# Kernel tuning notes

Measured on AMD Instinct MI355X. Metric: run time of the kernel, lower is better.

## Reference

```python
import jax, jax.numpy as jnp
import numpy as np

L, H, NH, FF = 12, 768, 12, 3072
HD = H // NH
B, T = 8, 512
SCALE = 1.0 / float(np.sqrt(HD))
EPS = 1e-12


def setup_inputs() -> dict:
    key = jax.random.key(0)
    ks = jax.random.split(key, 10)
    s = jnp.float32(0.02)

    def p(k, shape):
        return jax.random.normal(k, shape, dtype=jnp.float32) * s

    return {
        "hidden_states": jax.random.normal(ks[0], (B, T, H), dtype=jnp.float32),
        "attention_mask": jnp.ones((B, T), dtype=jnp.float32),
        "Wq": p(ks[1], (L, H, H)), "bq": jnp.zeros((L, H), jnp.float32),
        "Wk": p(ks[2], (L, H, H)), "bk": jnp.zeros((L, H), jnp.float32),
        "Wv": p(ks[3], (L, H, H)), "bv": jnp.zeros((L, H), jnp.float32),
        "Wao": p(ks[4], (L, H, H)), "bao": jnp.zeros((L, H), jnp.float32),
        "ln1_g": jnp.ones((L, H), jnp.float32), "ln1_b": jnp.zeros((L, H), jnp.float32),
        "Wi": p(ks[5], (L, H, FF)), "bi": jnp.zeros((L, FF), jnp.float32),
        "Wo": p(ks[6], (L, FF, H)), "bo": jnp.zeros((L, H), jnp.float32),
        "ln2_g": jnp.ones((L, H), jnp.float32), "ln2_b": jnp.zeros((L, H), jnp.float32),
    }


def _layernorm(x, g, b):
    m = jnp.mean(x, axis=-1, keepdims=True)
    v = jnp.mean((x - m) ** 2, axis=-1, keepdims=True)
    return (x - m) * jax.lax.rsqrt(v + EPS) * g + b


def _encoder(hidden_states, attention_mask, params):
    # additive mask: (1 - mask) * -10000, broadcast to [B, 1, 1, T]
    add_mask = (1.0 - attention_mask)[:, None, None, :] * -10000.0

    def layer(x, p):
        wq, bq, wk, bk, wv, bv, wao, bao, g1, b1, wi, bi, wo, bo, g2, b2 = p
        q = (x @ wq + bq).reshape(B, T, NH, HD)
        k = (x @ wk + bk).reshape(B, T, NH, HD)
        v = (x @ wv + bv).reshape(B, T, NH, HD)
        scores = jnp.einsum('bihd,bjhd->bhij', q, k) * SCALE + add_mask
        probs = jax.nn.softmax(scores, axis=-1)  # dropout p=0 (eval)
        ctx = jnp.einsum('bhij,bjhd->bihd', probs, v).reshape(B, T, H)
        attn_out = _layernorm(ctx @ wao + bao + x, g1, b1)
        ff = jax.nn.gelu(attn_out @ wi + bi, approximate=False)
        out = _layernorm(ff @ wo + bo + attn_out, g2, b2)
        return out, None

    out, _ = jax.lax.scan(layer, hidden_states, params)
    return out


def reference(hidden_states, attention_mask, Wq, bq, Wk, bk, Wv, bv, Wao, bao,
              ln1_g, ln1_b, Wi, bi, Wo, bo, ln2_g, ln2_b):
    params = (Wq, bq, Wk, bk, Wv, bv, Wao, bao, ln1_g, ln1_b, Wi, bi, Wo, bo, ln2_g, ln2_b)
    return _encoder(hidden_states, attention_mask, params)
```

## Files before the change

### kernel.cpp

```cpp
#include <hip/hip_runtime.h>
#include <hip/hip_bf16.h>

typedef __bf16 bf16;
typedef __attribute__((ext_vector_type(8))) __bf16 bf16x8;
typedef __attribute__((ext_vector_type(4))) float f32x4;

#define MFMA16(a, b, c) __builtin_amdgcn_mfma_f32_16x16x32_bf16((a), (b), (c), 0, 0, 0)

__device__ __forceinline__ void async16(const bf16* g, bf16* l) {
    __builtin_amdgcn_global_load_lds((__attribute__((address_space(1))) void*)(g),
                                     (__attribute__((address_space(3))) void*)(l), 16, 0, 0);
}

__device__ __forceinline__ void xcd_swizzle(int& bx, int& by, int& bz) {
    const int gx = gridDim.x, gy = gridDim.y;
    const int nwg = gx * gy * gridDim.z;
    const int lin = blockIdx.x + gx * (blockIdx.y + gy * blockIdx.z);
    const int xcd = lin & 7, seq = lin >> 3;
    const int q = nwg >> 3, r = nwg & 7;
    const int nl = (xcd < r ? xcd * (q + 1) : r * (q + 1) + (xcd - r) * q) + seq;
    bx = nl % gx;
    const int t = nl / gx;
    by = t % gy;
    bz = t / gy;
}

template <int MODE, int BM>
__global__ __launch_bounds__(256) void gemm_kernel(
    const bf16* __restrict__ A, const bf16* __restrict__ WT,
    const float* __restrict__ b0, const float* __restrict__ b1, const float* __restrict__ b2,
    int s1, int s2,
    void* __restrict__ o0, void* __restrict__ o1,
    int N, int K, int Kpart)
{
    constexpr int MT = BM / 32;
    __shared__ __align__(16) bf16 sA[2][BM * 32];
    __shared__ __align__(16) bf16 sB[2][128 * 32];

    const int tid  = threadIdx.x;
    const int lane = tid & 63;
    const int wave = tid >> 6;
    const int quad = lane >> 4;
    const int l15  = lane & 15;
    const int wm   = (wave >> 1) * (BM / 2);
    const int wn   = (wave & 1) * 64;

    int bxs, bys, bzs;
    xcd_swizzle(bxs, bys, bzs);
    const int bm = bys * BM;
    const int bn = bxs * 128;
    const int kbase = bzs * Kpart;

    f32x4 acc[MT][4];
#pragma unroll
    for (int i = 0; i < MT; i++)
#pragma unroll
        for (int j = 0; j < 4; j++)
#pragma unroll
            for (int r = 0; r < 4; r++) acc[i][j][r] = 0.0f;

    const int idx1 = tid + 256;
    const int ra0 = tid  >> 2, ca0 = (tid  & 3) * 8;
    const int rb1 = idx1 >> 2, cb1 = (idx1 & 3) * 8;

    const bf16* Arow0 = A  + (size_t)(bm + ra0) * K + kbase + ca0;
    const bf16* Arow1 = A  + (size_t)(bm + rb1) * K + kbase + cb1;
    const bf16* Brow0 = WT + (size_t)(bn + ra0) * K + kbase + ca0;
    const bf16* Brow1 = WT + (size_t)(bn + rb1) * K + kbase + cb1;

    const int nk = Kpart >> 5;

    async16(Arow0, sA[0] + tid * 8);
    if (BM == 128) async16(Arow1, sA[0] + idx1 * 8);
    async16(Brow0, sB[0] + tid * 8);
    async16(Brow1, sB[0] + idx1 * 8);
    __syncthreads();

    int cur = 0;
    for (int kt = 0; kt < nk; kt++) {
        if (kt + 1 < nk) {
            const int ko = (kt + 1) * 32;
            async16(Arow0 + ko, sA[cur ^ 1] + tid * 8);
            if (BM == 128) async16(Arow1 + ko, sA[cur ^ 1] + idx1 * 8);
            async16(Brow0 + ko, sB[cur ^ 1] + tid * 8);
            async16(Brow1 + ko, sB[cur ^ 1] + idx1 * 8);
        }
        bf16x8 af[MT], bfr[4];
#pragma unroll
        for (int i = 0; i < MT; i++)
            af[i] = *(const bf16x8*)(sA[cur] + (wm + i * 16 + l15) * 32 + quad * 8);
#pragma unroll
        for (int i = 0; i < 4; i++)
            bfr[i] = *(const bf16x8*)(sB[cur] + (wn + i * 16 + l15) * 32 + quad * 8);
#pragma unroll
        for (int mt = 0; mt < MT; mt++)
#pragma unroll
            for (int nt = 0; nt < 4; nt++)
                acc[mt][nt] = MFMA16(af[mt], bfr[nt], acc[mt][nt]);
        __syncthreads();
        cur ^= 1;
    }

    void* outp = (bzs == 0) ? o0 : o1;

#pragma unroll
    for (int nt = 0; nt < 4; nt++) {
        const int col = bn + wn + nt * 16 + l15;
        float bias = 0.0f;
        if (MODE != 1)
            bias = (col < s1) ? b0[col] : (col < s2) ? b1[col - s1] : b2[col - s2];
#pragma unroll
        for (int mt = 0; mt < MT; mt++) {
#pragma unroll
            for (int r = 0; r < 4; r++) {
                const int row = bm + wm + mt * 16 + quad * 4 + r;
                float v = acc[mt][nt][r] + bias;
                if (MODE == 2) v = 0.5f * v * (1.0f + erff(v * 0.70710678118654752f));
                if (MODE == 1) ((float*)outp)[(size_t)row * N + col] = v;
                else           ((bf16*)outp)[(size_t)row * N + col] = (bf16)v;
            }
        }
    }
}

__global__ __launch_bounds__(256) void vtrans_kernel(
    const bf16* __restrict__ qkv, bf16* __restrict__ vT)
{
    const int bh = blockIdx.y;
    const int b = bh / 12, h = bh - b * 12;
    const int k0 = blockIdx.x * 128;
    __shared__ __align__(16) bf16 tile[128 * 72];
    const int tid = threadIdx.x;
    const bf16* src = qkv + (size_t)(b * 512 + k0) * 2304 + 1536 + h * 64;
#pragma unroll
    for (int i = 0; i < 4; i++) {
        const int idx = i * 256 + tid;
        const int r = idx >> 3, c = (idx & 7) * 8;
        *(uint4*)(tile + r * 72 + c) = *(const uint4*)(src + (size_t)r * 2304 + c);
    }
    __syncthreads();
    bf16* dst = vT + (size_t)bh * 64 * 512 + k0;
#pragma unroll
    for (int i = 0; i < 4; i++) {
        const int idx = i * 256 + tid;
        const int d = idx & 63, kg = idx >> 6;
        alignas(16) bf16 tmp[8];
#pragma unroll
        for (int e = 0; e < 8; e++) tmp[e] = tile[(kg * 8 + e) * 72 + d];
        *(uint4*)(dst + (size_t)d * 512 + kg * 8) = *(uint4*)tmp;
    }
}

__global__ __launch_bounds__(256) void attn_kernel(
    const bf16* __restrict__ qkv, const bf16* __restrict__ vT,
    const float* __restrict__ mask, bf16* __restrict__ ctx)
{
    int bxs, bys, bzs;
    xcd_swizzle(bxs, bys, bzs);
    const int b = bzs, h = bys, q0 = bxs * 32;
    const int bh = b * 12 + h;
    const int tid = threadIdx.x, lane = tid & 63, wave = tid >> 6;
    const int quad = lane >> 4, l15 = lane & 15;
    const int mt = wave & 1;
    const int whi = wave >> 1;

    __shared__ __align__(16) bf16 sQ[32 * 80];
    __shared__ __align__(16) bf16 sKV[64 * 80];
    __shared__ __align__(16) bf16 sS[32 * 520];
    __shared__ float sAM[512];
    __shared__ float sRedM[32 * 8];
    __shared__ float sRedS[32 * 8];
    __shared__ float sRow[32];

    for (int i = tid; i < 512; i += 256)
        sAM[i] = (1.0f - mask[b * 512 + i]) * -10000.0f;

    const size_t RS = 2304;
    {
        const int r = tid >> 3, c = (tid & 7) * 8;
        *(uint4*)(sQ + r * 80 + c) =
            *(const uint4*)(qkv + (size_t)(b * 512 + q0 + r) * RS + h * 64 + c);
    }

#pragma unroll 1
    for (int kt = 0; kt < 8; kt++) {
        __syncthreads();
        const bf16* Kb = qkv + (size_t)(b * 512 + kt * 64) * RS + 768 + h * 64;
#pragma unroll
        for (int i = 0; i < 2; i++) {
            const int idx = i * 256 + tid;
            const int r = idx >> 3, c = (idx & 7) * 8;
            *(uint4*)(sKV + r * 80 + c) = *(const uint4*)(Kb + (size_t)r * RS + c);
        }
        __syncthreads();
        bf16x8 aQ0 = *(const bf16x8*)(sQ + (mt * 16 + l15) * 80 + quad * 8);
        bf16x8 aQ1 = *(const bf16x8*)(sQ + (mt * 16 + l15) * 80 + 32 + quad * 8);
#pragma unroll
        for (int n = 0; n < 2; n++) {
            const int nt = whi * 2 + n;
            f32x4 accS;
#pragma unroll
            for (int r = 0; r < 4; r++) accS[r] = 0.0f;
            accS = MFMA16(aQ0, *(const bf16x8*)(sKV + (nt * 16 + l15) * 80 + quad * 8), accS);
            accS = MFMA16(aQ1, *(const bf16x8*)(sKV + (nt * 16 + l15) * 80 + 32 + quad * 8), accS);
#pragma unroll
            for (int r = 0; r < 4; r++) {
                const int row = mt * 16 + quad * 4 + r;
                sS[row * 520 + kt * 64 + nt * 16 + l15] = (bf16)accS[r];
            }
        }
    }
    __syncthreads();

    {
        const int r = tid >> 3, p = tid & 7;
        float mx = -1e30f;
#pragma unroll
        for (int t = 0; t < 8; t++) {
            const int v0 = (p + 8 * t) * 8;
            bf16x8 pv = *(const bf16x8*)(sS + r * 520 + v0);
#pragma unroll
            for (int e = 0; e < 8; e++)
                mx = fmaxf(mx, (float)pv[e] * 0.125f + sAM[v0 + e]);
        }
        sRedM[r * 8 + p] = mx;
        __syncthreads();
#pragma unroll
        for (int q = 0; q < 8; q++) mx = fmaxf(mx, sRedM[r * 8 + q]);
        float sum = 0.0f;
#pragma unroll
        for (int t = 0; t < 8; t++) {
            const int v0 = (p + 8 * t) * 8;
            bf16x8 pv = *(const bf16x8*)(sS + r * 520 + v0);
            bf16x8 ev;
#pragma unroll
            for (int e = 0; e < 8; e++) {
                const float x = __expf((float)pv[e] * 0.125f + sAM[v0 + e] - mx);
                sum += x;
                ev[e] = (bf16)x;
            }
            *(bf16x8*)(sS + r * 520 + v0) = ev;
        }
        sRedS[r * 8 + p] = sum;
        __syncthreads();
        if (p == 0) {
            float s = 0.0f;
#pragma unroll
            for (int q = 0; q < 8; q++) s += sRedS[r * 8 + q];
            sRow[r] = s;
        }
    }

    f32x4 accO[2];
#pragma unroll
    for (int i = 0; i < 2; i++)
#pragma unroll
        for (int r = 0; r < 4; r++) accO[i][r] = 0.0f;

#pragma unroll 1
    for (int kt = 0; kt < 8; kt++) {
        __syncthreads();
        const bf16* Vt = vT + (size_t)bh * 64 * 512 + kt * 64;
#pragma unroll
        for (int i = 0; i < 2; i++) {
            const int idx = i * 256 + tid;
            const int r = idx >> 3, c = (idx & 7) * 8;
            *(uint4*)(sKV + r * 80 + c) = *(const uint4*)(Vt + (size_t)r * 512 + c);
        }
        __syncthreads();
#pragma unroll
        for (int kk = 0; kk < 2; kk++) {
            bf16x8 aP = *(const bf16x8*)(sS + (mt * 16 + l15) * 520 + kt * 64 + kk * 32 + quad * 8);
#pragma unroll
            for (int n = 0; n < 2; n++) {
                bf16x8 bV = *(const bf16x8*)(sKV + (whi * 32 + n * 16 + l15) * 80 + kk * 32 + quad * 8);
                accO[n] = MFMA16(aP, bV, accO[n]);
            }
        }
    }
#pragma unroll
    for (int n = 0; n < 2; n++) {
#pragma unroll
        for (int r = 0; r < 4; r++) {
            const int row = mt * 16 + quad * 4 + r;
            const float o = accO[n][r] / sRow[row];
            ctx[(size_t)(b * 512 + q0 + row) * 768 + h * 64 + whi * 32 + n * 16 + l15] = (bf16)o;
        }
    }
}

template <int NP>
__global__ __launch_bounds__(256) void ln_kernel(
    const float* __restrict__ p0, const float* __restrict__ p1,
    const float* __restrict__ bias, const float* __restrict__ resid,
    const float* __restrict__ g, const float* __restrict__ bb,
    bf16* __restrict__ out_bf, float* __restrict__ out_f32)
{
    const int row = blockIdx.x;
    const int tid = threadIdx.x;
    __shared__ float sS[4], sQ[4];

    float x[3], s = 0.0f, sq = 0.0f;
#pragma unroll
    for (int j = 0; j < 3; j++) {
        const int c = tid + j * 256;
        const size_t idx = (size_t)row * 768 + c;
        float v = p0[idx] + bias[c] + resid[idx];
        if (NP > 1) v += p1[idx];
        x[j] = v; s += v; sq += v * v;
    }
#pragma unroll
    for (int off = 32; off; off >>= 1) { s += __shfl_down(s, off); sq += __shfl_down(sq, off); }
    if ((tid & 63) == 0) { sS[tid >> 6] = s; sQ[tid >> 6] = sq; }
    __syncthreads();
    s  = sS[0] + sS[1] + sS[2] + sS[3];
    sq = sQ[0] + sQ[1] + sQ[2] + sQ[3];
    const float mean = s * (1.0f / 768.0f);
    float var = sq * (1.0f / 768.0f) - mean * mean;
    var = fmaxf(var, 0.0f);
    const float rstd = rsqrtf(var + 1e-12f);
#pragma unroll
    for (int j = 0; j < 3; j++) {
        const int c = tid + j * 256;
        const float v = (x[j] - mean) * rstd * g[c] + bb[c];
        out_bf[(size_t)row * 768 + c] = (bf16)v;
        out_f32[(size_t)row * 768 + c] = v;
    }
}

__global__ __launch_bounds__(256) void transpose_kernel(
    const float* __restrict__ Wq, const float* __restrict__ Wk, const float* __restrict__ Wv,
    const float* __restrict__ Wao, const float* __restrict__ Wi, const float* __restrict__ Wo,
    bf16* __restrict__ wT)
{
    __shared__ bf16 tile[64 * 68];
    int id = blockIdx.x;
    const float* src; bf16* dst; int Kd, Nd;
    if (id < 576) {
        const int w = id / 144; id -= w * 144;
        Kd = 768; Nd = 768;
        src = (w == 0) ? Wq : (w == 1) ? Wk : (w == 2) ? Wv : Wao;
        dst = wT + (size_t)w * 589824;
    } else if (id < 1152) {
        id -= 576; Kd = 768; Nd = 3072; src = Wi; dst = wT + 2359296;
    } else {
        id -= 1152; Kd = 3072; Nd = 768; src = Wo; dst = wT + 4718592;
    }
    const int tn = Nd >> 6;
    const int tr = id / tn, tc = id - tr * tn;
    const int r0 = tr * 64, c0 = tc * 64;
    const int tid = threadIdx.x;

#pragma unroll
    for (int i = 0; i < 4; i++) {
        const int idx = i * 256 + tid;
        const int r = idx >> 4, c4 = (idx & 15) * 4;
        const float4 f = *(const float4*)(src + (size_t)(r0 + r) * Nd + c0 + c4);
        alignas(8) bf16 q[4] = {(bf16)f.x, (bf16)f.y, (bf16)f.z, (bf16)f.w};
        *(ushort4*)(tile + r * 68 + c4) = *(ushort4*)q;
    }
    __syncthreads();
#pragma unroll
    for (int i = 0; i < 4; i++) {
        const int idx = i * 256 + tid;
        const int n = idx >> 4, kc = (idx & 15) * 4;
        alignas(8) bf16 tmp[4];
#pragma unroll
        for (int e = 0; e < 4; e++) tmp[e] = tile[(kc + e) * 68 + n];
        *(ushort4*)(dst + (size_t)(c0 + n) * Kd + r0 + kc) = *(ushort4*)tmp;
    }
}

__global__ __launch_bounds__(256) void convert_kernel(
    const float* __restrict__ in, bf16* __restrict__ out, int n)
{
    const int i = blockIdx.x * 256 + threadIdx.x;
    if (i < n) out[i] = (bf16)in[i];
}

extern "C" void kernel_launch(void* const* d_in, const int* in_sizes, int n_in,
                              void* d_out, int out_size, void* d_ws, size_t ws_size,
                              hipStream_t stream)
{
    const float* hidden = (const float*)d_in[0];
    const float* mask   = (const float*)d_in[1];
    const float* Wq  = (const float*)d_in[2];  const float* bq  = (const float*)d_in[3];
    const float* Wk  = (const float*)d_in[4];  const float* bk  = (const float*)d_in[5];
    const float* Wv  = (const float*)d_in[6];  const float* bv  = (const float*)d_in[7];
    const float* Wao = (const float*)d_in[8];  const float* bao = (const float*)d_in[9];
    const float* g1  = (const float*)d_in[10]; const float* be1 = (const float*)d_in[11];
    const float* Wi  = (const float*)d_in[12]; const float* bi  = (const float*)d_in[13];
    const float* Wo  = (const float*)d_in[14]; const float* bo  = (const float*)d_in[15];
    const float* g2  = (const float*)d_in[16]; const float* be2 = (const float*)d_in[17];

    char* ws = (char*)d_ws;
    bf16*  wT    = (bf16*)(ws);
    bf16*  qkv   = (bf16*)(ws + 14155776);
    bf16*  vT    = (bf16*)(ws + 33030144);
    bf16*  ctx   = (bf16*)(ws + 39321600);
    bf16*  attnb = (bf16*)(ws + 45613056);
    bf16*  xb    = (bf16*)(ws + 51904512);
    float* xf    = (float*)(ws + 58195968);
    float* attnf = (float*)(ws + 70778880);
    bf16*  ffh   = (bf16*)(ws + 14155776);
    float* pA0   = (float*)(ws + 14155776);
    float* pF0   = (float*)(ws + 39321600);
    float* pF1   = (float*)(ws + 83361792);

    convert_kernel<<<12288, 256, 0, stream>>>(hidden, xb, 3145728);

    for (int l = 0; l < 12; l++) {
        transpose_kernel<<<1728, 256, 0, stream>>>(
            Wq + (size_t)l * 589824, Wk + (size_t)l * 589824, Wv + (size_t)l * 589824,
            Wao + (size_t)l * 589824, Wi + (size_t)l * 2359296, Wo + (size_t)l * 2359296, wT);

        gemm_kernel<0, 64><<<dim3(18, 64, 1), 256, 0, stream>>>(
            xb, wT, bq + l * 768, bk + l * 768, bv + l * 768, 768, 1536,
            qkv, nullptr, 2304, 768, 768);

        vtrans_kernel<<<dim3(4, 96), 256, 0, stream>>>(qkv, vT);

        attn_kernel<<<dim3(16, 12, 8), 256, 0, stream>>>(qkv, vT, mask, ctx);

        gemm_kernel<1, 64><<<dim3(6, 64, 1), 256, 0, stream>>>(
            ctx, wT + 1769472, nullptr, nullptr, nullptr, 0, 0,
            pA0, nullptr, 768, 768, 768);

        const float* resid1 = (l == 0) ? hidden : xf;
        ln_kernel<1><<<4096, 256, 0, stream>>>(
            pA0, nullptr, bao + l * 768, resid1, g1 + l * 768, be1 + l * 768, attnb, attnf);

        gemm_kernel<2, 128><<<dim3(24, 32, 1), 256, 0, stream>>>(
            attnb, wT + 2359296, bi + l * 3072, bi + l * 3072, bi + l * 3072, 3072, 3072,
            ffh, nullptr, 3072, 768, 768);

        gemm_kernel<1, 64><<<dim3(6, 64, 2), 256, 0, stream>>>(
            ffh, wT + 4718592, nullptr, nullptr, nullptr, 0, 0,
            pF0, pF1, 768, 3072, 1536);

        float* f32dst = (l == 11) ? (float*)d_out : xf;
        ln_kernel<2><<<4096, 256, 0, stream>>>(
            pF0, pF1, bo + l * 768, attnf, g2 + l * 768, be2 + l * 768, xb, f32dst);
    }
}
```

Baseline: 2.513 ms.

## Double-buffer K/V tiles with async LDS loads and swizzle GEMM shared memory

The attention kernel now streams K and V tiles into double-buffered LDS with direct global-to-LDS async loads and an XOR swizzle, prefetching the next tile while the current one is consumed. Q fragments are loaded straight into registers. The GEMM drops __syncthreads in favour of explicit vmcnt/lgkmcnt waits plus barriers, and applies an XOR column swizzle to avoid LDS bank conflicts. This targets load latency and bank conflicts, at the cost of relying on hand-counted waitcnt values staying correct.

New measurement: 2.462 ms. -2.0%, faster.

```diff
diff --git a/kernel.cpp b/kernel.cpp
--- a/kernel.cpp
+++ b/kernel.cpp
@@ -6,6 +6,11 @@
 typedef __attribute__((ext_vector_type(4))) float f32x4;
 
 #define MFMA16(a, b, c) __builtin_amdgcn_mfma_f32_16x16x32_bf16((a), (b), (c), 0, 0, 0)
+
+#define SYNC_VM(N) do { asm volatile("s_waitcnt vmcnt(" #N ")" ::: "memory"); \
+    __builtin_amdgcn_s_barrier(); __builtin_amdgcn_sched_barrier(0); } while (0)
+#define SYNC_LGKM() do { asm volatile("s_waitcnt lgkmcnt(0)" ::: "memory"); \
+    __builtin_amdgcn_s_barrier(); __builtin_amdgcn_sched_barrier(0); } while (0)
 
 __device__ __forceinline__ void async16(const bf16* g, bf16* l) {
     __builtin_amdgcn_global_load_lds((__attribute__((address_space(1))) void*)(g),
@@ -60,11 +65,11 @@
             for (int r = 0; r < 4; r++) acc[i][j][r] = 0.0f;
 
     const int idx1 = tid + 256;
-    const int ra0 = tid  >> 2, ca0 = (tid  & 3) * 8;
-    const int rb1 = idx1 >> 2, cb1 = (idx1 & 3) * 8;
-
-    const bf16* Arow0 = A  + (size_t)(bm + ra0) * K + kbase + ca0;
-    const bf16* Arow1 = A  + (size_t)(bm + rb1) * K + kbase + cb1;
+    const int ra0 = tid >> 2,  ca0 = (((tid  & 3) ^ ((ra0 >> 1) & 3)) * 8);
+    const int rb1 = idx1 >> 2, cb1 = (((idx1 & 3) ^ ((rb1 >> 1) & 3)) * 8);
+
+    const bf16* Arow0 = A + (size_t)(bm + ra0) * K + kbase + ca0;
+    const bf16* Arow1 = (BM == 128) ? A + (size_t)(bm + rb1) * K + kbase + cb1 : A;
     const bf16* Brow0 = WT + (size_t)(bn + ra0) * K + kbase + ca0;
     const bf16* Brow1 = WT + (size_t)(bn + rb1) * K + kbase + cb1;
 
@@ -74,7 +79,8 @@
     if (BM == 128) async16(Arow1, sA[0] + idx1 * 8);
     async16(Brow0, sB[0] + tid * 8);
     async16(Brow1, sB[0] + idx1 * 8);
-    __syncthreads();
+
+    const int chF = (quad ^ ((l15 >> 1) & 3)) * 8;
 
     int cur = 0;
     for (int kt = 0; kt < nk; kt++) {
@@ -84,20 +90,24 @@
             if (BM == 128) async16(Arow1 + ko, sA[cur ^ 1] + idx1 * 8);
             async16(Brow0 + ko, sB[cur ^ 1] + tid * 8);
             async16(Brow1 + ko, sB[cur ^ 1] + idx1 * 8);
+            if (BM == 128) SYNC_VM(4);
+            else           SYNC_VM(3);
+        } else {
+            SYNC_VM(0);
         }
         bf16x8 af[MT], bfr[4];
 #pragma unroll
         for (int i = 0; i < MT; i++)
-            af[i] = *(const bf16x8*)(sA[cur] + (wm + i * 16 + l15) * 32 + quad * 8);
+            af[i] = *(const bf16x8*)(sA[cur] + (wm + i * 16 + l15) * 32 + chF);
 #pragma unroll
         for (int i = 0; i < 4; i++)
-            bfr[i] = *(const bf16x8*)(sB[cur] + (wn + i * 16 + l15) * 32 + quad * 8);
+            bfr[i] = *(const bf16x8*)(sB[cur] + (wn + i * 16 + l15) * 32 + chF);
 #pragma unroll
         for (int mt = 0; mt < MT; mt++)
 #pragma unroll
             for (int nt = 0; nt < 4; nt++)
                 acc[mt][nt] = MFMA16(af[mt], bfr[nt], acc[mt][nt]);
-        __syncthreads();
+        SYNC_LGKM();
         cur ^= 1;
     }
 
@@ -164,53 +174,64 @@
     const int mt = wave & 1;
     const int whi = wave >> 1;
 
-    __shared__ __align__(16) bf16 sQ[32 * 80];
-    __shared__ __align__(16) bf16 sKV[64 * 80];
+    __shared__ __align__(16) bf16 sKV[2][64 * 64];
     __shared__ __align__(16) bf16 sS[32 * 520];
     __shared__ float sAM[512];
-    __shared__ float sRedM[32 * 8];
-    __shared__ float sRedS[32 * 8];
+    __shared__ float sRed[256];
     __shared__ float sRow[32];
 
     for (int i = tid; i < 512; i += 256)
         sAM[i] = (1.0f - mask[b * 512 + i]) * -10000.0f;
 
     const size_t RS = 2304;
-    {
-        const int r = tid >> 3, c = (tid & 7) * 8;
-        *(uint4*)(sQ + r * 80 + c) =
-            *(const uint4*)(qkv + (size_t)(b * 512 + q0 + r) * RS + h * 64 + c);
-    }
-
-#pragma unroll 1
+    const bf16* Qrow = qkv + (size_t)(b * 512 + q0 + mt * 16 + l15) * RS + h * 64;
+    const bf16x8 aQ0 = *(const bf16x8*)(Qrow + quad * 8);
+    const bf16x8 aQ1 = *(const bf16x8*)(Qrow + 32 + quad * 8);
+
+    const int c0 = tid, c1 = tid + 256;
+    const int r0 = c0 >> 3, r1 = c1 >> 3;
+    const int sc0 = ((c0 & 7) ^ (r0 & 7)) * 8;
+    const int sc1 = ((c1 & 7) ^ (r1 & 7)) * 8;
+
+    const bf16* Kbase = qkv + (size_t)(b * 512) * RS + 768 + h * 64;
+
+    async16(Kbase + (size_t)(r0) * RS + sc0, (bf16*)sKV[0] + c0 * 8);
+    async16(Kbase + (size_t)(r1) * RS + sc1, (bf16*)sKV[0] + c1 * 8);
+
+#pragma unroll
     for (int kt = 0; kt < 8; kt++) {
-        __syncthreads();
-        const bf16* Kb = qkv + (size_t)(b * 512 + kt * 64) * RS + 768 + h * 64;
-#pragma unroll
-        for (int i = 0; i < 2; i++) {
-            const int idx = i * 256 + tid;
-            const int r = idx >> 3, c = (idx & 7) * 8;
-            *(uint4*)(sKV + r * 80 + c) = *(const uint4*)(Kb + (size_t)r * RS + c);
-        }
-        __syncthreads();
-        bf16x8 aQ0 = *(const bf16x8*)(sQ + (mt * 16 + l15) * 80 + quad * 8);
-        bf16x8 aQ1 = *(const bf16x8*)(sQ + (mt * 16 + l15) * 80 + 32 + quad * 8);
+        const int cur = kt & 1;
+        if (kt < 7) {
+            async16(Kbase + (size_t)((kt + 1) * 64 + r0) * RS + sc0, (bf16*)sKV[cur ^ 1] + c0 * 8);
+            async16(Kbase + (size_t)((kt + 1) * 64 + r1) * RS + sc1, (bf16*)sKV[cur ^ 1] + c1 * 8);
+            SYNC_VM(2);
+        } else {
+            SYNC_VM(0);
+        }
 #pragma unroll
         for (int n = 0; n < 2; n++) {
             const int nt = whi * 2 + n;
+            const int krow = nt * 16 + l15;
+            const int sw = krow & 7;
+            bf16x8 bK0 = *(const bf16x8*)(sKV[cur] + krow * 64 + ((quad ^ sw) * 8));
+            bf16x8 bK1 = *(const bf16x8*)(sKV[cur] + krow * 64 + (((4 + quad) ^ sw) * 8));
             f32x4 accS;
 #pragma unroll
             for (int r = 0; r < 4; r++) accS[r] = 0.0f;
-            accS = MFMA16(aQ0, *(const bf16x8*)(sKV + (nt * 16 + l15) * 80 + quad * 8), accS);
-            accS = MFMA16(aQ1, *(const bf16x8*)(sKV + (nt * 16 + l15) * 80 + 32 + quad * 8), accS);
+            accS = MFMA16(aQ0, bK0, accS);
+            accS = MFMA16(aQ1, bK1, accS);
 #pragma unroll
             for (int r = 0; r < 4; r++) {
                 const int row = mt * 16 + quad * 4 + r;
                 sS[row * 520 + kt * 64 + nt * 16 + l15] = (bf16)accS[r];
             }
         }
-    }
-    __syncthreads();
+        SYNC_LGKM();
+    }
+
+    const bf16* Vbase = vT + (size_t)bh * 64 * 512;
+    async16(Vbase + (size_t)r0 * 512 + sc0, (bf16*)sKV[0] + c0 * 8);
+    async16(Vbase + (size_t)r1 * 512 + sc1, (bf16*)sKV[0] + c1 * 8);
 
     {
         const int r = tid >> 3, p = tid & 7;
@@ -223,10 +244,10 @@
             for (int e = 0; e < 8; e++)
                 mx = fmaxf(mx, (float)pv[e] * 0.125f + sAM[v0 + e]);
         }
-        sRedM[r * 8 + p] = mx;
-        __syncthreads();
-#pragma unroll
-        for (int q = 0; q < 8; q++) mx = fmaxf(mx, sRedM[r * 8 + q]);
+        sRed[r * 8 + p] = mx;
+        SYNC_LGKM();
+#pragma unroll
+        for (int q = 0; q < 8; q++) mx = fmaxf(mx, sRed[r * 8 + q]);
         float sum = 0.0f;
 #pragma unroll
         for (int t = 0; t < 8; t++) {
@@ -241,12 +262,13 @@
             }
             *(bf16x8*)(sS + r * 520 + v0) = ev;
         }
-        sRedS[r * 8 + p] = sum;
-        __syncthreads();
+        SYNC_LGKM();
+        sRed[r * 8 + p] = sum;
+        SYNC_LGKM();
         if (p == 0) {
             float s = 0.0f;
 #pragma unroll
-            for (int q = 0; q < 8; q++) s += sRedS[r * 8 + q];
+            for (int q = 0; q < 8; q++) s += sRed[r * 8 + q];
             sRow[r] = s;
         }
     }
@@ -257,26 +279,27 @@
 #pragma unroll
         for (int r = 0; r < 4; r++) accO[i][r] = 0.0f;
 
-#pragma unroll 1
+#pragma unroll
     for (int kt = 0; kt < 8; kt++) {
-        __syncthreads();
-        const bf16* Vt = vT + (size_t)bh * 64 * 512 + kt * 64;
-#pragma unroll
-        for (int i = 0; i < 2; i++) {
-            const int idx = i * 256 + tid;
-            const int r = idx >> 3, c = (idx & 7) * 8;
-            *(uint4*)(sKV + r * 80 + c) = *(const uint4*)(Vt + (size_t)r * 512 + c);
-        }
-        __syncthreads();
+        const int cur = kt & 1;
+        if (kt < 7) {
+            async16(Vbase + (size_t)r0 * 512 + (kt + 1) * 64 + sc0, (bf16*)sKV[cur ^ 1] + c0 * 8);
+            async16(Vbase + (size_t)r1 * 512 + (kt + 1) * 64 + sc1, (bf16*)sKV[cur ^ 1] + c1 * 8);
+            SYNC_VM(2);
+        } else {
+            SYNC_VM(0);
+        }
 #pragma unroll
         for (int kk = 0; kk < 2; kk++) {
             bf16x8 aP = *(const bf16x8*)(sS + (mt * 16 + l15) * 520 + kt * 64 + kk * 32 + quad * 8);
 #pragma unroll
             for (int n = 0; n < 2; n++) {
-                bf16x8 bV = *(const bf16x8*)(sKV + (whi * 32 + n * 16 + l15) * 80 + kk * 32 + quad * 8);
+                const int vrow = whi * 32 + n * 16 + l15;
+                bf16x8 bV = *(const bf16x8*)(sKV[cur] + vrow * 64 + (((kk * 4 + quad) ^ (vrow & 7)) * 8));
                 accO[n] = MFMA16(aP, bV, accO[n]);
             }
         }
+        SYNC_LGKM();
     }
 #pragma unroll
     for (int n = 0; n < 2; n++) {
```
